# Performance work log

Hardware: AMD Instinct MI355X
Metric: run time of the kernel (lower is better)

The kernel has to match this reference:

```python
import jax, jax.numpy as jnp
import numpy as np

EMBED_DIM = 768
NUM_HEADS = 12
HEAD_DIM = EMBED_DIM // NUM_HEADS


def setup_inputs() -> dict:
    key = jax.random.key(0)
    ks = jax.random.split(key, 9)
    B, S, D = 2, 2048, EMBED_DIM
    scale = 1.0 / np.sqrt(D)
    x = jax.random.normal(ks[0], (B, S, D), dtype=jnp.float32)
    Wq = jax.random.normal(ks[1], (D, D), dtype=jnp.float32) * scale
    bq = jax.random.normal(ks[2], (D,), dtype=jnp.float32) * 0.01
    Wk = jax.random.normal(ks[3], (D, D), dtype=jnp.float32) * scale
    bk = jax.random.normal(ks[4], (D,), dtype=jnp.float32) * 0.01
    Wv = jax.random.normal(ks[5], (D, D), dtype=jnp.float32) * scale
    bv = jax.random.normal(ks[6], (D,), dtype=jnp.float32) * 0.01
    Wo = jax.random.normal(ks[7], (D, D), dtype=jnp.float32) * scale
    bo = jax.random.normal(ks[8], (D,), dtype=jnp.float32) * 0.01
    return {"x": x, "Wq": Wq, "bq": bq, "Wk": Wk, "bk": bk,
            "Wv": Wv, "bv": bv, "Wo": Wo, "bo": bo}


def reference(x, Wq, bq, Wk, bk, Wv, bv, Wo, bo):
    B, S, D = x.shape
    H, Dh = NUM_HEADS, HEAD_DIM
    # separate QKV projections (weights stored [in, out] so y = x @ W + b)
    q = (x @ Wq + bq).reshape(B, S, H, Dh)
    k = (x @ Wk + bk).reshape(B, S, H, Dh)
    v = (x @ Wv + bv).reshape(B, S, H, Dh)
    # NOTE: original module applies NO 1/sqrt(head_dim) scaling
    scores = jnp.einsum('bqhd,bkhd->bhqk', q, k)          # [B,H,S,S] materialized
    attn = jax.nn.softmax(scores, axis=-1)
    ctx = jnp.einsum('bhqk,bkhd->bqhd', attn, v)          # [B,S,H,Dh]
    out = ctx.reshape(B, S, D) @ Wo + bo
    return out
```

## Files before the change

kernel.cpp:

```cpp
#include <hip/hip_runtime.h>
#include <hip/hip_bf16.h>


typedef __attribute__((ext_vector_type(8))) short short8;
typedef __attribute__((ext_vector_type(4))) float float4e;

__device__ __forceinline__ ushort f2bf(float f) {
    union { float f; unsigned u; } v; v.f = f;
    unsigned r = v.u + 0x7FFF + ((v.u >> 16) & 1);
    return (ushort)(r >> 16);
}

__device__ __forceinline__ void async_cp16(const ushort* g, ushort* l) {
    __builtin_amdgcn_global_load_lds(
        (const __attribute__((address_space(1))) unsigned int*)g,
        (__attribute__((address_space(3))) unsigned int*)l,
        16, 0, 0);
}

__global__ __launch_bounds__(256) void cast_f32_bf16(
    const float* __restrict__ in, ushort* __restrict__ out, int n4)
{
    int i = blockIdx.x * blockDim.x + threadIdx.x;
    if (i < n4) {
        float4 v = *(const float4*)&in[(size_t)i * 4];
        ushort4 o;
        o.x = f2bf(v.x); o.y = f2bf(v.y); o.z = f2bf(v.z); o.w = f2bf(v.w);
        *(ushort4*)&out[(size_t)i * 4] = o;
    }
}

__global__ __launch_bounds__(256) void transpose_cast_w4(
    const float* __restrict__ W0, const float* __restrict__ W1,
    const float* __restrict__ W2, const float* __restrict__ W3,
    ushort* __restrict__ WtBase)
{
    __shared__ float t[64][65];
    const int z = blockIdx.z;
    const float* W = (z == 0) ? W0 : (z == 1) ? W1 : (z == 2) ? W2 : W3;
    ushort* Wt = WtBase + (size_t)z * (768u * 768u);

    const int tid = threadIdx.x;
    const int c  = tid & 63;
    const int rg = tid >> 6;
    const int k0 = blockIdx.y * 64, n0 = blockIdx.x * 64;
    #pragma unroll
    for (int r = 0; r < 16; ++r) {
        const int row = rg * 16 + r;
        t[row][c] = W[(size_t)(k0 + row) * 768 + n0 + c];
    }
    __syncthreads();
    #pragma unroll
    for (int r = 0; r < 16; ++r) {
        const int row = rg * 16 + r;
        Wt[(size_t)(n0 + row) * 768 + k0 + c] = f2bf(t[c][row]);
    }
}

__global__ __launch_bounds__(256) void transpose_v(
    const ushort* __restrict__ Vb, ushort* __restrict__ VT)
{
    __shared__ ushort t[64][72];
    const int tid = threadIdx.x;
    const int b = blockIdx.z, h = blockIdx.y, s0 = blockIdx.x * 64;
    const int lr = tid >> 3;
    const int lc = (tid & 7) * 8;

    #pragma unroll
    for (int half = 0; half < 64; half += 32) {
        const int row = lr + half;
        *(uint4*)&t[row][lc] =
            *(const uint4*)&Vb[(size_t)(b * 2048 + s0 + row) * 768 + h * 64 + lc];
    }
    __syncthreads();
    #pragma unroll
    for (int half = 0; half < 64; half += 32) {
        const int d = lr + half;
        ushort tmp[8];
        #pragma unroll
        for (int i = 0; i < 8; ++i) tmp[i] = t[lc + i][d];
        *(uint4*)&VT[((size_t)(b * 12 + h) * 64 + d) * 2048 + s0 + lc] =
            *(const uint4*)tmp;
    }
}

__global__ __launch_bounds__(256) void gemm_qkv_fused(
    const ushort* __restrict__ A, const ushort* __restrict__ Bt,
    const float* __restrict__ bq, const float* __restrict__ bk,
    const float* __restrict__ bv, ushort* __restrict__ Outbase)
{
    constexpr int K = 768;
    __shared__ ushort As[128][32];
    __shared__ ushort Bs[128][32];

    const int tid  = threadIdx.x;
    const int w    = tid >> 6;
    const int lane = tid & 63;
    const int l16  = lane & 15;
    const int quad = lane >> 4;
    const int wr   = (w >> 1) * 64;
    const int wc   = (w & 1) * 64;
    const int row0 = blockIdx.y * 128, col0 = blockIdx.x * 128;

    const int r4 = lane >> 2;
    const int c8 = (lane & 3) * 8;

    float4e acc[4][4];
    #pragma unroll
    for (int mi = 0; mi < 4; ++mi)
        #pragma unroll
        for (int ni = 0; ni < 4; ++ni) acc[mi][ni] = (float4e){0.f,0.f,0.f,0.f};

    for (int k0 = 0; k0 < K; k0 += 32) {
        #pragma unroll
        for (int i = 0; i < 2; ++i) {
            const int rr = w * 32 + i * 16;
            async_cp16(&A [(size_t)(row0 + rr + r4) * K + k0 + c8], &As[rr][0]);
            async_cp16(&Bt[(size_t)(col0 + rr + r4) * K + k0 + c8], &Bs[rr][0]);
        }
        __syncthreads();

        short8 af[4], bf[4];
        #pragma unroll
        for (int i = 0; i < 4; ++i) {
            af[i] = *(const short8*)&As[wr + i * 16 + l16][quad * 8];
            bf[i] = *(const short8*)&Bs[wc + i * 16 + l16][quad * 8];
        }
        #pragma unroll
        for (int mi = 0; mi < 4; ++mi)
            #pragma unroll
            for (int ni = 0; ni < 4; ++ni)
                acc[mi][ni] = __builtin_amdgcn_mfma_f32_16x16x32_bf16(
                    af[mi], bf[ni], acc[mi][ni], 0, 0, 0);
        __syncthreads();
    }

    const int seg = (col0 >= 1536) ? 2 : (col0 >= 768 ? 1 : 0);
    const float* bias = (seg == 0) ? bq : (seg == 1) ? bk : bv;
    const int ncol0 = col0 - seg * 768 + wc;
    ushort* outp = Outbase + (size_t)seg * (4096u * 768u);

    #pragma unroll
    for (int ni = 0; ni < 4; ++ni) {
        const int col = ncol0 + ni * 16 + l16;
        const float bs = bias[col];
        #pragma unroll
        for (int mi = 0; mi < 4; ++mi) {
            #pragma unroll
            for (int r = 0; r < 4; ++r) {
                const int row = row0 + wr + mi * 16 + quad * 4 + r;
                outp[(size_t)row * 768 + col] = f2bf(acc[mi][ni][r] + bs);
            }
        }
    }
}

__global__ __launch_bounds__(256) void gemm_wo_128(
    const ushort* __restrict__ A, const ushort* __restrict__ Bt,
    const float* __restrict__ bias, float* __restrict__ Cout)
{
    constexpr int K = 768, N = 768;
    __shared__ ushort As[128][40];
    __shared__ ushort Bs[128][40];

    const int tid  = threadIdx.x;
    const int w    = tid >> 6;
    const int lane = tid & 63;
    const int l16  = lane & 15;
    const int quad = lane >> 4;
    const int wr   = (w >> 1) * 64;
    const int wc   = (w & 1) * 64;
    const int row0 = blockIdx.y * 128, col0 = blockIdx.x * 128;
    const int sr = tid >> 2, sc = (tid & 3) * 8;

    float4e acc[4][4];
    #pragma unroll
    for (int mi = 0; mi < 4; ++mi)
        #pragma unroll
        for (int ni = 0; ni < 4; ++ni) acc[mi][ni] = (float4e){0.f,0.f,0.f,0.f};

    uint4 a0 = *(const uint4*)&A [(size_t)(row0 + sr     ) * K + sc];
    uint4 a1 = *(const uint4*)&A [(size_t)(row0 + sr + 64) * K + sc];
    uint4 b0 = *(const uint4*)&Bt[(size_t)(col0 + sr     ) * K + sc];
    uint4 b1 = *(const uint4*)&Bt[(size_t)(col0 + sr + 64) * K + sc];

    for (int k0 = 0; k0 < K; k0 += 32) {
        *(uint4*)&As[sr     ][sc] = a0;
        *(uint4*)&As[sr + 64][sc] = a1;
        *(uint4*)&Bs[sr     ][sc] = b0;
        *(uint4*)&Bs[sr + 64][sc] = b1;
        __syncthreads();

        if (k0 + 32 < K) {
            const int kn = k0 + 32;
            a0 = *(const uint4*)&A [(size_t)(row0 + sr     ) * K + kn + sc];
            a1 = *(const uint4*)&A [(size_t)(row0 + sr + 64) * K + kn + sc];
            b0 = *(const uint4*)&Bt[(size_t)(col0 + sr     ) * K + kn + sc];
            b1 = *(const uint4*)&Bt[(size_t)(col0 + sr + 64) * K + kn + sc];
        }

        short8 af[4], bf[4];
        #pragma unroll
        for (int i = 0; i < 4; ++i) {
            af[i] = *(const short8*)&As[wr + i * 16 + l16][quad * 8];
            bf[i] = *(const short8*)&Bs[wc + i * 16 + l16][quad * 8];
        }
        #pragma unroll
        for (int mi = 0; mi < 4; ++mi)
            #pragma unroll
            for (int ni = 0; ni < 4; ++ni)
                acc[mi][ni] = __builtin_amdgcn_mfma_f32_16x16x32_bf16(
                    af[mi], bf[ni], acc[mi][ni], 0, 0, 0);
        __syncthreads();
    }

    #pragma unroll
    for (int ni = 0; ni < 4; ++ni) {
        const int col = col0 + wc + ni * 16 + l16;
        const float bs = bias[col];
        #pragma unroll
        for (int mi = 0; mi < 4; ++mi) {
            #pragma unroll
            for (int r = 0; r < 4; ++r) {
                const int row = row0 + wr + mi * 16 + quad * 4 + r;
                Cout[(size_t)row * N + col] = acc[mi][ni][r] + bs;
            }
        }
    }
}

__global__ __launch_bounds__(256) void attn_mfma(
    const ushort* __restrict__ Qg, const ushort* __restrict__ Kgl,
    const ushort* __restrict__ VT, ushort* __restrict__ Ctx)
{
    constexpr int S = 2048, D = 768;
    __shared__ ushort Ks [64][72];
    __shared__ ushort Vts[64][72];
    __shared__ ushort Ps [64][72];

    const int tid  = threadIdx.x;
    const int w    = tid >> 6;
    const int lane = tid & 63;
    const int l16  = lane & 15;
    const int quad = lane >> 4;
    const int b = blockIdx.z, h = blockIdx.y, q0 = blockIdx.x * 64;
    const size_t hc = (size_t)h * 64;

    const size_t qoff = (size_t)(b * S + q0 + w * 16 + l16) * D + hc + quad * 8;
    const short8 yq0 = *(const short8*)&Qg[qoff];
    const short8 yq1 = *(const short8*)&Qg[qoff + 32];

    float m_ = -1e30f, l_ = 0.f;
    float4e oa[4];
    #pragma unroll
    for (int n = 0; n < 4; ++n) oa[n] = (float4e){0.f, 0.f, 0.f, 0.f};

    const int sr = tid >> 2;
    const int sc = (tid & 3) * 16;
    const size_t vtb = ((size_t)(b * 12 + h) * 64 + sr) * 2048;

    uint4 kA, kB, vA, vB;
    {
        const size_t gk = (size_t)(b * S + sr) * D + hc + sc;
        kA = *(const uint4*)&Kgl[gk];
        kB = *(const uint4*)&Kgl[gk + 8];
        vA = *(const uint4*)&VT[vtb + sc];
        vB = *(const uint4*)&VT[vtb + sc + 8];
    }

    for (int k0 = 0; k0 < S; k0 += 64) {
        *(uint4*)&Ks [sr][sc    ] = kA;
        *(uint4*)&Ks [sr][sc + 8] = kB;
        *(uint4*)&Vts[sr][sc    ] = vA;
        *(uint4*)&Vts[sr][sc + 8] = vB;
        __syncthreads();

        if (k0 + 64 < S) {
            const size_t gk = (size_t)(b * S + k0 + 64 + sr) * D + hc + sc;
            kA = *(const uint4*)&Kgl[gk];
            kB = *(const uint4*)&Kgl[gk + 8];
            vA = *(const uint4*)&VT[vtb + k0 + 64 + sc];
            vB = *(const uint4*)&VT[vtb + k0 + 64 + sc + 8];
        }

        float4e sa[4];
        #pragma unroll
        for (int kb = 0; kb < 4; ++kb) {
            const short8 xk0 = *(const short8*)&Ks[kb * 16 + l16][quad * 8];
            const short8 xk1 = *(const short8*)&Ks[kb * 16 + l16][32 + quad * 8];
            float4e z = (float4e){0.f, 0.f, 0.f, 0.f};
            z      = __builtin_amdgcn_mfma_f32_16x16x32_bf16(xk0, yq0, z, 0, 0, 0);
            sa[kb] = __builtin_amdgcn_mfma_f32_16x16x32_bf16(xk1, yq1, z, 0, 0, 0);
        }

        float mx = -1e30f;
        #pragma unroll
        for (int kb = 0; kb < 4; ++kb)
            #pragma unroll
            for (int r = 0; r < 4; ++r) mx = fmaxf(mx, sa[kb][r]);
        mx = fmaxf(mx, __shfl_xor(mx, 16, 64));
        mx = fmaxf(mx, __shfl_xor(mx, 32, 64));
        const float mn = fmaxf(m_, mx);
        const float alpha = __expf(m_ - mn);
        float p[4][4], ps = 0.f;
        #pragma unroll
        for (int kb = 0; kb < 4; ++kb)
            #pragma unroll
            for (int r = 0; r < 4; ++r) {
                p[kb][r] = __expf(sa[kb][r] - mn);
                ps += p[kb][r];
            }
        ps += __shfl_xor(ps, 16, 64);
        ps += __shfl_xor(ps, 32, 64);
        l_ = l_ * alpha + ps;
        m_ = mn;

        #pragma unroll
        for (int kb = 0; kb < 4; ++kb) {
            ushort4 pk;
            pk.x = f2bf(p[kb][0]); pk.y = f2bf(p[kb][1]);
            pk.z = f2bf(p[kb][2]); pk.w = f2bf(p[kb][3]);
            *(ushort4*)&Ps[w * 16 + l16][kb * 16 + quad * 4] = pk;
        }

        #pragma unroll
        for (int n = 0; n < 4; ++n)
            #pragma unroll
            for (int r = 0; r < 4; ++r) oa[n][r] *= alpha;

        const short8 yp0 = *(const short8*)&Ps[w * 16 + l16][quad * 8];
        const short8 yp1 = *(const short8*)&Ps[w * 16 + l16][32 + quad * 8];
        #pragma unroll
        for (int db = 0; db < 4; ++db) {
            const short8 xv0 = *(const short8*)&Vts[db * 16 + l16][quad * 8];
            const short8 xv1 = *(const short8*)&Vts[db * 16 + l16][32 + quad * 8];
            oa[db] = __builtin_amdgcn_mfma_f32_16x16x32_bf16(xv0, yp0, oa[db], 0, 0, 0);
            oa[db] = __builtin_amdgcn_mfma_f32_16x16x32_bf16(xv1, yp1, oa[db], 0, 0, 0);
        }
        __syncthreads();
    }

    const float inv = 1.0f / l_;
    const size_t crow = (size_t)(b * S + q0 + w * 16 + l16) * D + hc;
    #pragma unroll
    for (int db = 0; db < 4; ++db) {
        ushort4 ov;
        ov.x = f2bf(oa[db][0] * inv); ov.y = f2bf(oa[db][1] * inv);
        ov.z = f2bf(oa[db][2] * inv); ov.w = f2bf(oa[db][3] * inv);
        *(ushort4*)&Ctx[crow + db * 16 + quad * 4] = ov;
    }
}

extern "C" void kernel_launch(void* const* d_in, const int* in_sizes, int n_in,
                              void* d_out, int out_size, void* d_ws, size_t ws_size,
                              hipStream_t stream)
{
    const float* x  = (const float*)d_in[0];
    const float* Wq = (const float*)d_in[1];
    const float* bq = (const float*)d_in[2];
    const float* Wk = (const float*)d_in[3];
    const float* bk = (const float*)d_in[4];
    const float* Wv = (const float*)d_in[5];
    const float* bv = (const float*)d_in[6];
    const float* Wo = (const float*)d_in[7];
    const float* bo = (const float*)d_in[8];

    const int M = 4096, D = 768;
    const size_t XE = (size_t)M * D;
    const size_t WE = (size_t)D * D;

    ushort* xb   = (ushort*)d_ws;
    ushort* wtq  = xb   + XE;
    ushort* wto  = wtq  + 3 * WE;
    ushort* qb   = wto  + WE;
    ushort* kb   = qb   + XE;
    ushort* vb   = kb   + XE;
    ushort* ctxb = vb   + XE;
    ushort* vt   = xb;

    cast_f32_bf16<<<(int)(XE / 4 / 256), 256, 0, stream>>>(x, xb, (int)(XE / 4));

    transpose_cast_w4<<<dim3(12, 12, 4), 256, 0, stream>>>(Wq, Wk, Wv, Wo, wtq);

    gemm_qkv_fused<<<dim3(2304 / 128, 4096 / 128), 256, 0, stream>>>(
        xb, wtq, bq, bk, bv, qb);

    transpose_v<<<dim3(32, 12, 2), 256, 0, stream>>>(vb, vt);

    attn_mfma<<<dim3(2048 / 64, 12, 2), 256, 0, stream>>>(qb, kb, vt, ctxb);

    gemm_wo_128<<<dim3(768 / 128, 4096 / 128), 256, 0, stream>>>(
        ctxb, wto, bo, (float*)d_out);
}
```

Measured before the change: 194.7 us.

## Merge cast kernels, use async LDS loads in Wo GEMM, pack bf16 conversions

New measurement: 198.0 us. Within noise of the previous version (+1.7%).

```diff
diff --git a/kernel.cpp b/kernel.cpp
--- a/kernel.cpp
+++ b/kernel.cpp
@@ -9,6 +9,13 @@
     union { float f; unsigned u; } v; v.f = f;
     unsigned r = v.u + 0x7FFF + ((v.u >> 16) & 1);
     return (ushort)(r >> 16);
+}
+
+__device__ __forceinline__ unsigned pk2bf(float a, float b) {
+    float2 t; t.x = a; t.y = b;
+    __hip_bfloat162 h = __float22bfloat162_rn(t);
+    union { __hip_bfloat162 h; unsigned u; } cv; cv.h = h;
+    return cv.u;
 }
 
 __device__ __forceinline__ void async_cp16(const ushort* g, ushort* l) {
@@ -18,29 +25,31 @@
         16, 0, 0);
 }
 
-__global__ __launch_bounds__(256) void cast_f32_bf16(
-    const float* __restrict__ in, ushort* __restrict__ out, int n4)
-{
-    int i = blockIdx.x * blockDim.x + threadIdx.x;
-    if (i < n4) {
-        float4 v = *(const float4*)&in[(size_t)i * 4];
-        ushort4 o;
-        o.x = f2bf(v.x); o.y = f2bf(v.y); o.z = f2bf(v.z); o.w = f2bf(v.w);
-        *(ushort4*)&out[(size_t)i * 4] = o;
-    }
-}
-
-__global__ __launch_bounds__(256) void transpose_cast_w4(
+__global__ __launch_bounds__(256) void prep_cast(
+    const float* __restrict__ x, ushort* __restrict__ xb,
     const float* __restrict__ W0, const float* __restrict__ W1,
     const float* __restrict__ W2, const float* __restrict__ W3,
     ushort* __restrict__ WtBase)
 {
     __shared__ float t[64][65];
     const int z = blockIdx.z;
+    const int tid = threadIdx.x;
+
+    if (z == 4) {
+        const int nblk = gridDim.x * gridDim.y;
+        const int bid  = blockIdx.y * gridDim.x + blockIdx.x;
+        const int n4   = 4096 * 768 / 4;
+        for (int i = bid * 256 + tid; i < n4; i += nblk * 256) {
+            float4 v = *(const float4*)&x[(size_t)i * 4];
+            ushort4 o;
+            o.x = f2bf(v.x); o.y = f2bf(v.y); o.z = f2bf(v.z); o.w = f2bf(v.w);
+            *(ushort4*)&xb[(size_t)i * 4] = o;
+        }
+        return;
+    }
+
     const float* W = (z == 0) ? W0 : (z == 1) ? W1 : (z == 2) ? W2 : W3;
     ushort* Wt = WtBase + (size_t)z * (768u * 768u);
-
-    const int tid = threadIdx.x;
     const int c  = tid & 63;
     const int rg = tid >> 6;
     const int k0 = blockIdx.y * 64, n0 = blockIdx.x * 64;
@@ -160,8 +169,8 @@
     const float* __restrict__ bias, float* __restrict__ Cout)
 {
     constexpr int K = 768, N = 768;
-    __shared__ ushort As[128][40];
-    __shared__ ushort Bs[128][40];
+    __shared__ ushort As[128][32];
+    __shared__ ushort Bs[128][32];
 
     const int tid  = threadIdx.x;
     const int w    = tid >> 6;
@@ -171,7 +180,9 @@
     const int wr   = (w >> 1) * 64;
     const int wc   = (w & 1) * 64;
     const int row0 = blockIdx.y * 128, col0 = blockIdx.x * 128;
-    const int sr = tid >> 2, sc = (tid & 3) * 8;
+
+    const int r4 = lane >> 2;
+    const int c8 = (lane & 3) * 8;
 
     float4e acc[4][4];
     #pragma unroll
@@ -179,25 +190,14 @@
         #pragma unroll
         for (int ni = 0; ni < 4; ++ni) acc[mi][ni] = (float4e){0.f,0.f,0.f,0.f};
 
-    uint4 a0 = *(const uint4*)&A [(size_t)(row0 + sr     ) * K + sc];
-    uint4 a1 = *(const uint4*)&A [(size_t)(row0 + sr + 64) * K + sc];
-    uint4 b0 = *(const uint4*)&Bt[(size_t)(col0 + sr     ) * K + sc];
-    uint4 b1 = *(const uint4*)&Bt[(size_t)(col0 + sr + 64) * K + sc];
-
     for (int k0 = 0; k0 < K; k0 += 32) {
-        *(uint4*)&As[sr     ][sc] = a0;
-        *(uint4*)&As[sr + 64][sc] = a1;
-        *(uint4*)&Bs[sr     ][sc] = b0;
-        *(uint4*)&Bs[sr + 64][sc] = b1;
-        __syncthreads();
-
-        if (k0 + 32 < K) {
-            const int kn = k0 + 32;
-            a0 = *(const uint4*)&A [(size_t)(row0 + sr     ) * K + kn + sc];
-            a1 = *(const uint4*)&A [(size_t)(row0 + sr + 64) * K + kn + sc];
-            b0 = *(const uint4*)&Bt[(size_t)(col0 + sr     ) * K + kn + sc];
-            b1 = *(const uint4*)&Bt[(size_t)(col0 + sr + 64) * K + kn + sc];
-        }
+        #pragma unroll
+        for (int i = 0; i < 2; ++i) {
+            const int rr = w * 32 + i * 16;
+            async_cp16(&A [(size_t)(row0 + rr + r4) * K + k0 + c8], &As[rr][0]);
+            async_cp16(&Bt[(size_t)(col0 + rr + r4) * K + k0 + c8], &Bs[rr][0]);
+        }
+        __syncthreads();
 
         short8 af[4], bf[4];
         #pragma unroll
@@ -317,10 +317,10 @@
 
         #pragma unroll
         for (int kb = 0; kb < 4; ++kb) {
-            ushort4 pk;
-            pk.x = f2bf(p[kb][0]); pk.y = f2bf(p[kb][1]);
-            pk.z = f2bf(p[kb][2]); pk.w = f2bf(p[kb][3]);
-            *(ushort4*)&Ps[w * 16 + l16][kb * 16 + quad * 4] = pk;
+            uint2 pk;
+            pk.x = pk2bf(p[kb][0], p[kb][1]);
+            pk.y = pk2bf(p[kb][2], p[kb][3]);
+            *(uint2*)&Ps[w * 16 + l16][kb * 16 + quad * 4] = pk;
         }
 
         #pragma unroll
@@ -344,10 +344,10 @@
     const size_t crow = (size_t)(b * S + q0 + w * 16 + l16) * D + hc;
     #pragma unroll
     for (int db = 0; db < 4; ++db) {
-        ushort4 ov;
-        ov.x = f2bf(oa[db][0] * inv); ov.y = f2bf(oa[db][1] * inv);
-        ov.z = f2bf(oa[db][2] * inv); ov.w = f2bf(oa[db][3] * inv);
-        *(ushort4*)&Ctx[crow + db * 16 + quad * 4] = ov;
+        uint2 ov;
+        ov.x = pk2bf(oa[db][0] * inv, oa[db][1] * inv);
+        ov.y = pk2bf(oa[db][2] * inv, oa[db][3] * inv);
+        *(uint2*)&Ctx[crow + db * 16 + quad * 4] = ov;
     }
 }
 
@@ -378,9 +378,7 @@
     ushort* ctxb = vb   + XE;
     ushort* vt   = xb;
 
-    cast_f32_bf16<<<(int)(XE / 4 / 256), 256, 0, stream>>>(x, xb, (int)(XE / 4));
-
-    transpose_cast_w4<<<dim3(12, 12, 4), 256, 0, stream>>>(Wq, Wk, Wv, Wo, wtq);
+    prep_cast<<<dim3(12, 12, 5), 256, 0, stream>>>(x, xb, Wq, Wk, Wv, Wo, wtq);
 
     gemm_qkv_fused<<<dim3(2304 / 128, 4096 / 128), 256, 0, stream>>>(
         xb, wtq, bq, bk, bv, qb);
```
